# Kernel optimization log

Hardware: AMD Instinct MI355X
Metric: run time of the kernel (lower is better)

The kernel has to match this reference:

```python
import jax, jax.numpy as jnp
import numpy as np

B, NQ, NC1, NC2 = 2, 1024, 1024, 1024
QD = CD1 = CD2 = 1024
H, DH = 8, 64
INNER = H * DH          # 512
VD = 1024               # v_dim, split across heads -> 128 per head
VDH = VD // H


def setup_inputs() -> dict:
    key = jax.random.key(0)
    ks = jax.random.split(key, 18)
    f = lambda k, shape: jax.random.normal(k, shape, jnp.float32) * 0.02
    return {
        "x": f(ks[0], (B, NQ, QD)),
        "context": f(ks[1], (B, NC1, CD1)),
        "context2": f(ks[2], (B, NC2, CD2)),
        "mask1": jax.random.uniform(ks[3], (B, NQ, NC1)) > 0.1,
        "mask2": jax.random.uniform(ks[4], (B, NQ, NC2)) > 0.1,
        "Wq": f(ks[5], (QD, INNER)),  "bq": f(ks[6], (INNER,)),
        "Wk1": f(ks[7], (CD1, INNER)), "bk1": f(ks[8], (INNER,)),
        "Wv1": f(ks[9], (CD1, VD)),    "bv1": f(ks[10], (VD,)),
        "Wk2": f(ks[11], (CD2, INNER)), "bk2": f(ks[12], (INNER,)),
        "Wv2": f(ks[13], (CD2, VD)),    "bv2": f(ks[14], (VD,)),
        "Wo": f(ks[15], (VD, VD)),      "bo": f(ks[16], (VD,)),
    }


def _split_heads(t, d):
    # b n (h d) -> b h n d
    b, n, _ = t.shape
    return t.reshape(b, n, H, d).transpose(0, 2, 1, 3)


def reference(x, context, context2, mask1, mask2,
              Wq, bq, Wk1, bk1, Wv1, bv1, Wk2, bk2, Wv2, bv2, Wo, bo):
    scale = DH ** -0.5
    q = x @ Wq + bq
    k = jnp.concatenate([context @ Wk1 + bk1, context2 @ Wk2 + bk2], axis=1)
    v = jnp.concatenate([context @ Wv1 + bv1, context2 @ Wv2 + bv2], axis=1)

    qh = _split_heads(q, DH)   # [B,H,NQ,DH]
    kh = _split_heads(k, DH)   # [B,H,NC1+NC2,DH]
    vh = _split_heads(v, VDH)  # [B,H,NC1+NC2,VDH]

    sim = jnp.einsum('bhid,bhjd->bhij', qh, kh) * scale  # [B,H,NQ,J]
    mask = jnp.concatenate([mask1, mask2], axis=2)[:, None, :, :]  # [B,1,NQ,J]
    max_neg = -jnp.finfo(sim.dtype).max
    sim = jnp.where(mask, sim, max_neg)

    attn = jax.nn.softmax(sim, axis=-1)
    out = jnp.einsum('bhij,bhjd->bhid', attn, vh)          # [B,H,NQ,VDH]
    out = out.transpose(0, 2, 1, 3).reshape(B, NQ, VD)     # b n (h d)
    return out @ Wo + bo
```

## Files before the change

kernel.cpp:

```cpp
#include <hip/hip_runtime.h>
#include <math.h>

typedef short bf16x8 __attribute__((ext_vector_type(8)));
typedef float f32x4  __attribute__((ext_vector_type(4)));

__device__ __forceinline__ unsigned short f2bf(float f) {
    unsigned int u = __builtin_bit_cast(unsigned int, f);
    u += 0x7FFFu + ((u >> 16) & 1u);
    return (unsigned short)(u >> 16);
}

__device__ __forceinline__ void gld16(const unsigned short* g, unsigned short* l) {
    __builtin_amdgcn_global_load_lds(
        (const __attribute__((address_space(1))) void*)g,
        (__attribute__((address_space(3))) void*)l, 16, 0, 0);
}

__global__ __launch_bounds__(256) void cast3(
    const float* __restrict__ a0, const float* __restrict__ a1, const float* __restrict__ a2,
    unsigned short* __restrict__ o0, unsigned short* __restrict__ o1, unsigned short* __restrict__ o2)
{
    const int z = blockIdx.z;
    const float* a = z == 0 ? a0 : (z == 1 ? a1 : a2);
    unsigned short* o = z == 0 ? o0 : (z == 1 ? o1 : o2);
    size_t i = ((size_t)blockIdx.x * 256 + threadIdx.x) * 8;
    float4 x0 = *(const float4*)&a[i];
    float4 x1 = *(const float4*)&a[i + 4];
    uint4 pk;
    pk.x = (unsigned)f2bf(x0.x) | ((unsigned)f2bf(x0.y) << 16);
    pk.y = (unsigned)f2bf(x0.z) | ((unsigned)f2bf(x0.w) << 16);
    pk.z = (unsigned)f2bf(x1.x) | ((unsigned)f2bf(x1.y) << 16);
    pk.w = (unsigned)f2bf(x1.z) | ((unsigned)f2bf(x1.w) << 16);
    *(uint4*)&o[i] = pk;
}

__global__ __launch_bounds__(256) void cast_t3(
    const float* __restrict__ W0, const float* __restrict__ W1, const float* __restrict__ W2,
    unsigned short* __restrict__ T0, unsigned short* __restrict__ T1, unsigned short* __restrict__ T2,
    int K, int N)
{
    __shared__ float T[64][65];
    const int z = blockIdx.z;
    const float* W = z == 0 ? W0 : (z == 1 ? W1 : W2);
    unsigned short* O = z == 0 ? T0 : (z == 1 ? T1 : T2);
    const int n0 = blockIdx.x << 6, k0 = blockIdx.y << 6;
    const int t = threadIdx.x;
    #pragma unroll
    for (int i = 0; i < 4; i++) {
        int vi = t + (i << 8);
        int r = vi >> 4, c4 = (vi & 15) << 2;
        *(float4*)&T[r][c4] = *(const float4*)&W[(size_t)(k0 + r) * N + n0 + c4];
    }
    __syncthreads();
    #pragma unroll
    for (int i = 0; i < 4; i++) {
        int vi = t + (i << 8);
        int n = vi >> 4, k4 = (vi & 15) << 2;
        uint2 pk;
        pk.x = (unsigned)f2bf(T[k4 + 0][n]) | ((unsigned)f2bf(T[k4 + 1][n]) << 16);
        pk.y = (unsigned)f2bf(T[k4 + 2][n]) | ((unsigned)f2bf(T[k4 + 3][n]) << 16);
        *(uint2*)&O[(size_t)(n0 + n) * K + k0 + k4] = pk;
    }
}

__global__ __launch_bounds__(256) void pack_mask(
    const int* __restrict__ mask1, const int* __restrict__ mask2,
    unsigned long long* __restrict__ mpk)
{
    int wid = (blockIdx.x << 2) + (threadIdx.x >> 6);
    int lane = threadIdx.x & 63;
    const int* m1 = mask1 + ((size_t)wid << 10);
    const int* m2 = mask2 + ((size_t)wid << 10);
    unsigned long long* o = mpk + ((size_t)wid << 5);
    #pragma unroll
    for (int win = 0; win < 16; win++) {
        unsigned long long bal = __ballot(m1[(win << 6) + lane] != 0);
        if (lane == 0) o[win] = bal;
    }
    #pragma unroll
    for (int win = 0; win < 16; win++) {
        unsigned long long bal = __ballot(m2[(win << 6) + lane] != 0);
        if (lane == 0) o[16 + win] = bal;
    }
}

__device__ __forceinline__ void gemm_core(
    const unsigned short* __restrict__ A,
    const unsigned short* __restrict__ Wt,
    int K, int gm0, int gn0,
    unsigned short (*As)[32], unsigned short (*Bs)[32],
    f32x4 (&acc)[4][4])
{
    const int t = threadIdx.x;
    const int lane = t & 63, w = t >> 6;
    const int wm = (w & 1) << 6, wn = (w >> 1) << 6;
    const int l15 = lane & 15, quad = lane >> 4;

    for (int k0 = 0; k0 < K; k0 += 32) {
        __syncthreads();
        #pragma unroll
        for (int i = 0; i < 2; i++) {
            int r0 = (i << 6) + (w << 4);
            int ra = r0 + (lane >> 2);
            int kc = (lane & 3) << 3;
            gld16(&A [(size_t)(gm0 + ra) * K + k0 + kc], &As[r0][0] + ((size_t)lane << 3));
            gld16(&Wt[(size_t)(gn0 + ra) * K + k0 + kc], &Bs[r0][0] + ((size_t)lane << 3));
        }
        __syncthreads();
        bf16x8 af[4], bg[4];
        #pragma unroll
        for (int i = 0; i < 4; i++)
            af[i] = *(const bf16x8*)&As[wm + (i << 4) + l15][quad << 3];
        #pragma unroll
        for (int j = 0; j < 4; j++)
            bg[j] = *(const bf16x8*)&Bs[wn + (j << 4) + l15][quad << 3];
        #pragma unroll
        for (int i = 0; i < 4; i++)
            #pragma unroll
            for (int j = 0; j < 4; j++)
                acc[i][j] = __builtin_amdgcn_mfma_f32_16x16x32_bf16(af[i], bg[j], acc[i][j], 0, 0, 0);
    }
}

__global__ __launch_bounds__(256) void proj_all(
    const unsigned short* __restrict__ xb, const unsigned short* __restrict__ c1b,
    const unsigned short* __restrict__ c2b,
    const unsigned short* __restrict__ Wqt, const unsigned short* __restrict__ Wk1t,
    const unsigned short* __restrict__ Wk2t, const unsigned short* __restrict__ Wv1t,
    const unsigned short* __restrict__ Wv2t,
    const float* __restrict__ bq, const float* __restrict__ bk1, const float* __restrict__ bk2,
    const float* __restrict__ bv1, const float* __restrict__ bv2,
    unsigned short* __restrict__ qbuf, unsigned short* __restrict__ kbuf,
    unsigned short* __restrict__ vbT)
{
    __shared__ unsigned short As[128][32];
    __shared__ unsigned short Bs[128][32];
    const int bid = blockIdx.x;
    int z, bx, by;
    if (bid < 192) { z = bid >> 6; int l = bid & 63; by = l >> 2; bx = l & 3; }
    else { int l = bid - 192; z = 3 + (l >> 7); l &= 127; by = l >> 3; bx = l & 7; }
    const unsigned short* A  = (z == 0) ? xb : (z == 1 || z == 3) ? c1b : c2b;
    const unsigned short* Wt = (z == 0) ? Wqt : (z == 1) ? Wk1t : (z == 2) ? Wk2t
                             : (z == 3) ? Wv1t : Wv2t;
    const float* bias = (z == 0) ? bq : (z == 1) ? bk1 : (z == 2) ? bk2
                      : (z == 3) ? bv1 : bv2;
    const int gm0 = by << 7, gn0 = bx << 7;

    f32x4 acc[4][4];
    #pragma unroll
    for (int i = 0; i < 4; i++)
        #pragma unroll
        for (int j = 0; j < 4; j++) acc[i][j] = (f32x4){0.f, 0.f, 0.f, 0.f};

    gemm_core(A, Wt, 1024, gm0, gn0, As, Bs, acc);

    const int lane = threadIdx.x & 63, w = threadIdx.x >> 6;
    const int wm = (w & 1) << 6, wn = (w >> 1) << 6;
    const int l15 = lane & 15, quad = lane >> 4;
    float bb[4];
    #pragma unroll
    for (int j = 0; j < 4; j++) bb[j] = bias[gn0 + wn + (j << 4) + l15];

    if (z < 3) {
        unsigned short* out = (z == 0) ? qbuf : kbuf;
        const int obs = (z == 0) ? 1024 : 2048;
        const int off = (z == 2) ? 1024 : 0;
        #pragma unroll
        for (int i = 0; i < 4; i++) {
            int mb = gm0 + wm + (i << 4) + (quad << 2);
            #pragma unroll
            for (int p = 0; p < 4; p++) {
                int m = mb + p;
                int orow = ((m >> 10) * obs) + off + (m & 1023);
                #pragma unroll
                for (int j = 0; j < 4; j++)
                    out[(size_t)orow * 512 + gn0 + wn + (j << 4) + l15] = f2bf(acc[i][j][p] + bb[j]);
            }
        }
    } else {
        const int off = (z == 3) ? 0 : 1024;
        #pragma unroll
        for (int i = 0; i < 4; i++) {
            int mb = gm0 + wm + (i << 4) + (quad << 2);
            int b = mb >> 10;
            int jj = (mb & 1023) + off;
            #pragma unroll
            for (int j = 0; j < 4; j++) {
                int n = gn0 + wn + (j << 4) + l15;
                unsigned long long pk = 0;
                #pragma unroll
                for (int p = 0; p < 4; p++)
                    pk |= (unsigned long long)f2bf(acc[i][j][p] + bb[j]) << (16 * p);
                *(unsigned long long*)&vbT[((size_t)b * 1024 + n) * 2048 + jj] = pk;
            }
        }
    }
}

__global__ __launch_bounds__(256) void gemm_out(
    const unsigned short* __restrict__ abuf, const unsigned short* __restrict__ Wot,
    const float* __restrict__ bo, float* __restrict__ out)
{
    __shared__ unsigned short As[128][32];
    __shared__ unsigned short Bs[128][32];
    const int gm0 = blockIdx.y << 7, gn0 = blockIdx.x << 7;

    f32x4 acc[4][4];
    #pragma unroll
    for (int i = 0; i < 4; i++)
        #pragma unroll
        for (int j = 0; j < 4; j++) acc[i][j] = (f32x4){0.f, 0.f, 0.f, 0.f};

    gemm_core(abuf, Wot, 1024, gm0, gn0, As, Bs, acc);

    const int lane = threadIdx.x & 63, w = threadIdx.x >> 6;
    const int wm = (w & 1) << 6, wn = (w >> 1) << 6;
    const int l15 = lane & 15, quad = lane >> 4;
    float bb[4];
    #pragma unroll
    for (int j = 0; j < 4; j++) bb[j] = bo[gn0 + wn + (j << 4) + l15];
    #pragma unroll
    for (int i = 0; i < 4; i++) {
        int mb = gm0 + wm + (i << 4) + (quad << 2);
        #pragma unroll
        for (int p = 0; p < 4; p++)
            #pragma unroll
            for (int j = 0; j < 4; j++)
                out[(size_t)(mb + p) * 1024 + gn0 + wn + (j << 4) + l15] = acc[i][j][p] + bb[j];
    }
}

__global__ __launch_bounds__(256) void attn_mfma(
    const unsigned short* __restrict__ qbuf, const unsigned short* __restrict__ kbuf,
    const unsigned short* __restrict__ vbT, const unsigned long long* __restrict__ mpk,
    float* __restrict__ Opart, float* __restrict__ ml)
{
    __shared__ unsigned short Ks[128][64];
    __shared__ unsigned short VsT[128][128];
    __shared__ unsigned short Ps[64][128];

    const int t = threadIdx.x;
    const int bid = blockIdx.x;
    const int hs = bid >> 8, r = bid & 255;
    const int h = r & 7, qt = (r >> 3) & 15, b = r >> 7;
    const int q0 = qt << 6;
    const int lane = t & 63, w = t >> 6, l15 = lane & 15, quad = lane >> 4;

    const unsigned short* qrow = qbuf + (((size_t)(b << 10) + q0 + (w << 4) + l15) << 9) + (h << 6);
    const bf16x8 aq0 = *(const bf16x8*)&qrow[quad << 3];
    const bf16x8 aq1 = *(const bf16x8*)&qrow[32 + (quad << 3)];

    f32x4 acc[8];
    #pragma unroll
    for (int ct = 0; ct < 8; ct++) acc[ct] = (f32x4){0.f, 0.f, 0.f, 0.f};
    float m_p[4] = {-3.0e38f, -3.0e38f, -3.0e38f, -3.0e38f};
    float l_p[4] = {0.f, 0.f, 0.f, 0.f};

    const size_t kbase = (size_t)b << 20;
    const size_t vbase = ((size_t)((b << 10) + (h << 7))) << 11;
    const int qg = q0 + (w << 4) + (quad << 2);
    const unsigned long long* mrow0 = mpk + (((size_t)(b << 10) + qg) << 5);

    for (int jt = 0; jt < 8; jt++) {
        const int j0 = (hs << 10) + (jt << 7);
        __syncthreads();
        #pragma unroll
        for (int i = 0; i < 4; i++) {
            int vi = t + (i << 8);
            int row = vi >> 3, c = vi & 7;
            *(uint4*)&Ks[row][(c ^ (row & 7)) << 3] =
                *(const uint4*)&kbuf[kbase + ((size_t)(j0 + row) << 9) + (h << 6) + (c << 3)];
        }
        #pragma unroll
        for (int i = 0; i < 8; i++) {
            int vi = t + (i << 8);
            int f = vi >> 4, c = vi & 15;
            int sc = (c & 8) | ((c & 7) ^ (f & 7));
            *(uint4*)&VsT[f][sc << 3] =
                *(const uint4*)&vbT[vbase + ((size_t)f << 11) + j0 + (c << 3)];
        }
        __syncthreads();

        f32x4 s[8];
        #pragma unroll
        for (int n = 0; n < 8; n++) {
            int rowk = (n << 4) + l15;
            bf16x8 bk0 = *(const bf16x8*)&Ks[rowk][(quad ^ (l15 & 7)) << 3];
            bf16x8 bk1 = *(const bf16x8*)&Ks[rowk][((quad | 4) ^ (l15 & 7)) << 3];
            s[n] = (f32x4){0.f, 0.f, 0.f, 0.f};
            s[n] = __builtin_amdgcn_mfma_f32_16x16x32_bf16(aq0, bk0, s[n], 0, 0, 0);
            s[n] = __builtin_amdgcn_mfma_f32_16x16x32_bf16(aq1, bk1, s[n], 0, 0, 0);
        }

        const int wbase = j0 >> 6;
        #pragma unroll
        for (int p = 0; p < 4; p++) {
            const unsigned long long* mr = mrow0 + ((size_t)p << 5);
            unsigned long long w0 = mr[wbase], w1 = mr[wbase + 1];
            #pragma unroll
            for (int n = 0; n < 8; n++) {
                unsigned long long wd = (n < 4) ? w0 : w1;
                int bit = ((n & 3) << 4) + l15;
                float sv = s[n][p] * 0.125f;
                s[n][p] = ((wd >> bit) & 1ull) ? sv : -3.0e38f;
            }
        }

        float alpha[4];
        #pragma unroll
        for (int p = 0; p < 4; p++) {
            float mt = s[0][p];
            #pragma unroll
            for (int n = 1; n < 8; n++) mt = fmaxf(mt, s[n][p]);
            #pragma unroll
            for (int o = 1; o < 16; o <<= 1) mt = fmaxf(mt, __shfl_xor(mt, o, 64));
            float mn = fmaxf(m_p[p], mt);
            float e[8], ls = 0.f;
            #pragma unroll
            for (int n = 0; n < 8; n++) { e[n] = __expf(s[n][p] - mn); ls += e[n]; }
            #pragma unroll
            for (int o = 1; o < 16; o <<= 1) ls += __shfl_xor(ls, o, 64);
            alpha[p] = __expf(m_p[p] - mn);
            l_p[p] = l_p[p] * alpha[p] + ls;
            m_p[p] = mn;
            int pr = (w << 4) + (quad << 2) + p;
            #pragma unroll
            for (int n = 0; n < 8; n++) {
                int c = (n << 1) + (l15 >> 3);
                int sc = (c & 8) | ((c & 7) ^ (pr & 7));
                Ps[pr][(sc << 3) + (l15 & 7)] = f2bf(e[n]);
            }
        }

        #pragma unroll
        for (int ct = 0; ct < 8; ct++)
            #pragma unroll
            for (int p = 0; p < 4; p++) acc[ct][p] *= alpha[p];

        bf16x8 ap[4];
        #pragma unroll
        for (int kk = 0; kk < 4; kk++) {
            int c = (kk << 2) + quad;
            int sc = (c & 8) | ((c & 7) ^ (l15 & 7));
            ap[kk] = *(const bf16x8*)&Ps[(w << 4) + l15][sc << 3];
        }
        #pragma unroll
        for (int ct = 0; ct < 8; ct++) {
            int fv = (ct << 4) + l15;
            #pragma unroll
            for (int kk = 0; kk < 4; kk++) {
                int c = (kk << 2) + quad;
                int sc = (c & 8) | ((c & 7) ^ (l15 & 7));
                bf16x8 bv = *(const bf16x8*)&VsT[fv][sc << 3];
                acc[ct] = __builtin_amdgcn_mfma_f32_16x16x32_bf16(ap[kk], bv, acc[ct], 0, 0, 0);
            }
        }
    }

    #pragma unroll
    for (int p = 0; p < 4; p++) {
        int q = q0 + (w << 4) + (quad << 2) + p;
        size_t idx = (size_t)(hs << 14) + (b << 13) + (h << 10) + q;
        #pragma unroll
        for (int ct = 0; ct < 8; ct++)
            Opart[(idx << 7) + (ct << 4) + l15] = acc[ct][p];
        if (l15 == 0) {
            ml[(idx << 1) + 0] = m_p[p];
            ml[(idx << 1) + 1] = l_p[p];
        }
    }
}

__global__ __launch_bounds__(256) void attn_combine(
    const float* __restrict__ Opart, const float* __restrict__ ml,
    unsigned short* __restrict__ abuf)
{
    int id = (blockIdx.x << 8) + threadIdx.x;
    int bhq = id >> 5, c4 = (id & 31) << 2;
    float2 ml0 = ((const float2*)ml)[bhq];
    float2 ml1 = ((const float2*)ml)[16384 + bhq];
    float M = fmaxf(ml0.x, ml1.x);
    float a0 = __expf(ml0.x - M), a1 = __expf(ml1.x - M);
    float inv = 1.0f / (ml0.y * a0 + ml1.y * a1);
    float4 o0 = *(const float4*)&Opart[((size_t)bhq << 7) + c4];
    float4 o1 = *(const float4*)&Opart[((size_t)(16384 + bhq) << 7) + c4];
    int b = bhq >> 13, hh = (bhq >> 10) & 7, q = bhq & 1023;
    float r0 = (o0.x * a0 + o1.x * a1) * inv;
    float r1 = (o0.y * a0 + o1.y * a1) * inv;
    float r2 = (o0.z * a0 + o1.z * a1) * inv;
    float r3 = (o0.w * a0 + o1.w * a1) * inv;
    unsigned long long pk = (unsigned long long)f2bf(r0)
        | ((unsigned long long)f2bf(r1) << 16)
        | ((unsigned long long)f2bf(r2) << 32)
        | ((unsigned long long)f2bf(r3) << 48);
    *(unsigned long long*)&abuf[((size_t)((b << 10) + q) << 10) + (hh << 7) + c4] = pk;
}

extern "C" void kernel_launch(void* const* d_in, const int* in_sizes, int n_in,
                              void* d_out, int out_size, void* d_ws, size_t ws_size,
                              hipStream_t stream)
{
    const float* x        = (const float*)d_in[0];
    const float* context  = (const float*)d_in[1];
    const float* context2 = (const float*)d_in[2];
    const int*   mask1    = (const int*)d_in[3];
    const int*   mask2    = (const int*)d_in[4];
    const float* Wq  = (const float*)d_in[5];
    const float* bq  = (const float*)d_in[6];
    const float* Wk1 = (const float*)d_in[7];
    const float* bk1 = (const float*)d_in[8];
    const float* Wv1 = (const float*)d_in[9];
    const float* bv1 = (const float*)d_in[10];
    const float* Wk2 = (const float*)d_in[11];
    const float* bk2 = (const float*)d_in[12];
    const float* Wv2 = (const float*)d_in[13];
    const float* bv2 = (const float*)d_in[14];
    const float* Wo  = (const float*)d_in[15];
    const float* bo  = (const float*)d_in[16];
    float* out = (float*)d_out;

    char* W = (char*)d_ws;
    unsigned short* Wot  = (unsigned short*)(W);
    unsigned short* xb   = (unsigned short*)(W + (2ull  << 20));
    unsigned short* c1b  = (unsigned short*)(W + (6ull  << 20));
    unsigned short* c2b  = (unsigned short*)(W + (10ull << 20));
    unsigned short* Wqt  = (unsigned short*)(W + (14ull << 20));
    unsigned short* Wk1t = (unsigned short*)(W + (15ull << 20));
    unsigned short* Wk2t = (unsigned short*)(W + (16ull << 20));
    unsigned short* Wv1t = (unsigned short*)(W + (17ull << 20));
    unsigned short* Wv2t = (unsigned short*)(W + (19ull << 20));
    unsigned short* qbuf = (unsigned short*)(W + (21ull << 20));
    unsigned short* kbuf = (unsigned short*)(W + (23ull << 20));
    unsigned short* vbT  = (unsigned short*)(W + (27ull << 20));
    float*              Opart = (float*)(W + (2ull << 20));
    unsigned long long* mpk   = (unsigned long long*)(W + (18ull << 20));
    float*              mlb   = (float*)(W + (18ull << 20) + (1ull << 19));
    unsigned short*     abuf  = (unsigned short*)(W + (19ull << 20));

    cast3   <<<dim3(1024, 1, 3), 256, 0, stream>>>(x, context, context2, xb, c1b, c2b);
    cast_t3 <<<dim3(8, 16, 3),   256, 0, stream>>>(Wq, Wk1, Wk2, Wqt, Wk1t, Wk2t, 1024, 512);
    cast_t3 <<<dim3(16, 16, 3),  256, 0, stream>>>(Wv1, Wv2, Wo, Wv1t, Wv2t, Wot, 1024, 1024);
    proj_all<<<dim3(448),        256, 0, stream>>>(xb, c1b, c2b, Wqt, Wk1t, Wk2t, Wv1t, Wv2t,
                                                   bq, bk1, bk2, bv1, bv2, qbuf, kbuf, vbT);
    pack_mask<<<dim3(512),       256, 0, stream>>>(mask1, mask2, mpk);
    attn_mfma<<<dim3(512),       256, 0, stream>>>(qbuf, kbuf, vbT, mpk, Opart, mlb);
    attn_combine<<<dim3(2048),   256, 0, stream>>>(Opart, mlb, abuf);
    gemm_out<<<dim3(8, 16),      256, 0, stream>>>(abuf, Wot, bo, out);
}
```

Before: 257.0 us.

## Transpose QK^T MFMA for lane-per-row softmax and narrow output GEMM tiles

The attention kernel swaps the MFMA operands so the S tile comes out transposed. Each lane then holds one query row's scores, so the row max and sum need only two cross-lane shuffles instead of four per row. P is written as packed 64-bit stores into a padded LDS array rather than scattered 16-bit stores, and the per-row rescale factors are fetched by shuffle. Separately, the output-projection GEMM is templated down to 128x64 tiles, doubling its block count to 256 so more CUs are busy, at the cost of more A-tile reloads.

```diff
diff --git a/kernel.cpp b/kernel.cpp
--- a/kernel.cpp
+++ b/kernel.cpp
@@ -84,16 +84,18 @@
     }
 }
 
+template<int NT>
 __device__ __forceinline__ void gemm_core(
     const unsigned short* __restrict__ A,
     const unsigned short* __restrict__ Wt,
     int K, int gm0, int gn0,
     unsigned short (*As)[32], unsigned short (*Bs)[32],
-    f32x4 (&acc)[4][4])
-{
+    f32x4 (&acc)[4][NT / 32])
+{
+    constexpr int NS = NT / 32;
     const int t = threadIdx.x;
     const int lane = t & 63, w = t >> 6;
-    const int wm = (w & 1) << 6, wn = (w >> 1) << 6;
+    const int wm = (w & 1) << 6, wn = (w >> 1) * (NT / 2);
     const int l15 = lane & 15, quad = lane >> 4;
 
     for (int k0 = 0; k0 < K; k0 += 32) {
@@ -103,21 +105,27 @@
             int r0 = (i << 6) + (w << 4);
             int ra = r0 + (lane >> 2);
             int kc = (lane & 3) << 3;
-            gld16(&A [(size_t)(gm0 + ra) * K + k0 + kc], &As[r0][0] + ((size_t)lane << 3));
+            gld16(&A[(size_t)(gm0 + ra) * K + k0 + kc], &As[r0][0] + ((size_t)lane << 3));
+        }
+        #pragma unroll
+        for (int i = 0; i < NT / 64; i++) {
+            int r0 = (i << 6) + (w << 4);
+            int ra = r0 + (lane >> 2);
+            int kc = (lane & 3) << 3;
             gld16(&Wt[(size_t)(gn0 + ra) * K + k0 + kc], &Bs[r0][0] + ((size_t)lane << 3));
         }
         __syncthreads();
-        bf16x8 af[4], bg[4];
+        bf16x8 af[4], bg[NS];
         #pragma unroll
         for (int i = 0; i < 4; i++)
             af[i] = *(const bf16x8*)&As[wm + (i << 4) + l15][quad << 3];
         #pragma unroll
-        for (int j = 0; j < 4; j++)
+        for (int j = 0; j < NS; j++)
             bg[j] = *(const bf16x8*)&Bs[wn + (j << 4) + l15][quad << 3];
         #pragma unroll
         for (int i = 0; i < 4; i++)
             #pragma unroll
-            for (int j = 0; j < 4; j++)
+            for (int j = 0; j < NS; j++)
                 acc[i][j] = __builtin_amdgcn_mfma_f32_16x16x32_bf16(af[i], bg[j], acc[i][j], 0, 0, 0);
     }
 }
@@ -152,7 +160,7 @@
         #pragma unroll
         for (int j = 0; j < 4; j++) acc[i][j] = (f32x4){0.f, 0.f, 0.f, 0.f};
 
-    gemm_core(A, Wt, 1024, gm0, gn0, As, Bs, acc);
+    gemm_core<128>(A, Wt, 1024, gm0, gn0, As, Bs, acc);
 
     const int lane = threadIdx.x & 63, w = threadIdx.x >> 6;
     const int wm = (w & 1) << 6, wn = (w >> 1) << 6;
@@ -202,30 +210,30 @@
     const float* __restrict__ bo, float* __restrict__ out)
 {
     __shared__ unsigned short As[128][32];
-    __shared__ unsigned short Bs[128][32];
-    const int gm0 = blockIdx.y << 7, gn0 = blockIdx.x << 7;
-
-    f32x4 acc[4][4];
+    __shared__ unsigned short Bs[64][32];
+    const int gm0 = blockIdx.y << 7, gn0 = blockIdx.x << 6;
+
+    f32x4 acc[4][2];
     #pragma unroll
     for (int i = 0; i < 4; i++)
         #pragma unroll
-        for (int j = 0; j < 4; j++) acc[i][j] = (f32x4){0.f, 0.f, 0.f, 0.f};
-
-    gemm_core(abuf, Wot, 1024, gm0, gn0, As, Bs, acc);
+        for (int j = 0; j < 2; j++) acc[i][j] = (f32x4){0.f, 0.f, 0.f, 0.f};
+
+    gemm_core<64>(abuf, Wot, 1024, gm0, gn0, As, Bs, acc);
 
     const int lane = threadIdx.x & 63, w = threadIdx.x >> 6;
-    const int wm = (w & 1) << 6, wn = (w >> 1) << 6;
+    const int wm = (w & 1) << 6, wn = (w >> 1) << 5;
     const int l15 = lane & 15, quad = lane >> 4;
-    float bb[4];
-    #pragma unroll
-    for (int j = 0; j < 4; j++) bb[j] = bo[gn0 + wn + (j << 4) + l15];
+    float bb[2];
+    #pragma unroll
+    for (int j = 0; j < 2; j++) bb[j] = bo[gn0 + wn + (j << 4) + l15];
     #pragma unroll
     for (int i = 0; i < 4; i++) {
         int mb = gm0 + wm + (i << 4) + (quad << 2);
         #pragma unroll
         for (int p = 0; p < 4; p++)
             #pragma unroll
-            for (int j = 0; j < 4; j++)
+            for (int j = 0; j < 2; j++)
                 out[(size_t)(mb + p) * 1024 + gn0 + wn + (j << 4) + l15] = acc[i][j][p] + bb[j];
     }
 }
@@ -237,7 +245,7 @@
 {
     __shared__ unsigned short Ks[128][64];
     __shared__ unsigned short VsT[128][128];
-    __shared__ unsigned short Ps[64][128];
+    __shared__ unsigned short Ps[64][132];
 
     const int t = threadIdx.x;
     const int bid = blockIdx.x;
@@ -253,13 +261,11 @@
     f32x4 acc[8];
     #pragma unroll
     for (int ct = 0; ct < 8; ct++) acc[ct] = (f32x4){0.f, 0.f, 0.f, 0.f};
-    float m_p[4] = {-3.0e38f, -3.0e38f, -3.0e38f, -3.0e38f};
-    float l_p[4] = {0.f, 0.f, 0.f, 0.f};
+    float m_l = -3.0e38f, l_l = 0.f;
 
     const size_t kbase = (size_t)b << 20;
     const size_t vbase = ((size_t)((b << 10) + (h << 7))) << 11;
-    const int qg = q0 + (w << 4) + (quad << 2);
-    const unsigned long long* mrow0 = mpk + (((size_t)(b << 10) + qg) << 5);
+    const unsigned long long* mrow = mpk + (((size_t)(b << 10) + q0 + (w << 4) + l15) << 5);
 
     for (int jt = 0; jt < 8; jt++) {
         const int j0 = (hs << 10) + (jt << 7);
@@ -288,71 +294,71 @@
             bf16x8 bk0 = *(const bf16x8*)&Ks[rowk][(quad ^ (l15 & 7)) << 3];
             bf16x8 bk1 = *(const bf16x8*)&Ks[rowk][((quad | 4) ^ (l15 & 7)) << 3];
             s[n] = (f32x4){0.f, 0.f, 0.f, 0.f};
-            s[n] = __builtin_amdgcn_mfma_f32_16x16x32_bf16(aq0, bk0, s[n], 0, 0, 0);
-            s[n] = __builtin_amdgcn_mfma_f32_16x16x32_bf16(aq1, bk1, s[n], 0, 0, 0);
+            s[n] = __builtin_amdgcn_mfma_f32_16x16x32_bf16(bk0, aq0, s[n], 0, 0, 0);
+            s[n] = __builtin_amdgcn_mfma_f32_16x16x32_bf16(bk1, aq1, s[n], 0, 0, 0);
         }
 
         const int wbase = j0 >> 6;
-        #pragma unroll
-        for (int p = 0; p < 4; p++) {
-            const unsigned long long* mr = mrow0 + ((size_t)p << 5);
-            unsigned long long w0 = mr[wbase], w1 = mr[wbase + 1];
-            #pragma unroll
-            for (int n = 0; n < 8; n++) {
-                unsigned long long wd = (n < 4) ? w0 : w1;
-                int bit = ((n & 3) << 4) + l15;
+        const unsigned long long w0 = mrow[wbase], w1 = mrow[wbase + 1];
+        #pragma unroll
+        for (int n = 0; n < 8; n++) {
+            unsigned long long wd = (n < 4) ? w0 : w1;
+            int bit0 = ((n & 3) << 4) + (quad << 2);
+            #pragma unroll
+            for (int p = 0; p < 4; p++) {
                 float sv = s[n][p] * 0.125f;
-                s[n][p] = ((wd >> bit) & 1ull) ? sv : -3.0e38f;
+                s[n][p] = ((wd >> (bit0 + p)) & 1ull) ? sv : -3.0e38f;
             }
         }
 
-        float alpha[4];
-        #pragma unroll
-        for (int p = 0; p < 4; p++) {
-            float mt = s[0][p];
-            #pragma unroll
-            for (int n = 1; n < 8; n++) mt = fmaxf(mt, s[n][p]);
-            #pragma unroll
-            for (int o = 1; o < 16; o <<= 1) mt = fmaxf(mt, __shfl_xor(mt, o, 64));
-            float mn = fmaxf(m_p[p], mt);
-            float e[8], ls = 0.f;
-            #pragma unroll
-            for (int n = 0; n < 8; n++) { e[n] = __expf(s[n][p] - mn); ls += e[n]; }
-            #pragma unroll
-            for (int o = 1; o < 16; o <<= 1) ls += __shfl_xor(ls, o, 64);
-            alpha[p] = __expf(m_p[p] - mn);
-            l_p[p] = l_p[p] * alpha[p] + ls;
-            m_p[p] = mn;
-            int pr = (w << 4) + (quad << 2) + p;
-            #pragma unroll
-            for (int n = 0; n < 8; n++) {
-                int c = (n << 1) + (l15 >> 3);
-                int sc = (c & 8) | ((c & 7) ^ (pr & 7));
-                Ps[pr][(sc << 3) + (l15 & 7)] = f2bf(e[n]);
-            }
-        }
-
+        float mt = s[0][0];
+        #pragma unroll
+        for (int n = 0; n < 8; n++)
+            #pragma unroll
+            for (int p = 0; p < 4; p++) mt = fmaxf(mt, s[n][p]);
+        mt = fmaxf(mt, __shfl_xor(mt, 16, 64));
+        mt = fmaxf(mt, __shfl_xor(mt, 32, 64));
+        float mn = fmaxf(m_l, mt);
+        float ls = 0.f;
+        #pragma unroll
+        for (int n = 0; n < 8; n++) {
+            float e0 = __expf(s[n][0] - mn), e1 = __expf(s[n][1] - mn);
+            float e2 = __expf(s[n][2] - mn), e3 = __expf(s[n][3] - mn);
+            ls += (e0 + e1) + (e2 + e3);
+            unsigned long long pk = (unsigned long long)f2bf(e0)
+                | ((unsigned long long)f2bf(e1) << 16)
+                | ((unsigned long long)f2bf(e2) << 32)
+                | ((unsigned long long)f2bf(e3) << 48);
+            *(unsigned long long*)&Ps[(w << 4) + l15][(n << 4) + (quad << 2)] = pk;
+        }
+        ls += __shfl_xor(ls, 16, 64);
+        ls += __shfl_xor(ls, 32, 64);
+        float al = __expf(m_l - mn);
+        l_l = l_l * al + ls;
+        m_l = mn;
+
+        float ar[4];
+        #pragma unroll
+        for (int p = 0; p < 4; p++)
+            ar[p] = __shfl(al, (lane & 48) | ((quad << 2) + p), 64);
         #pragma unroll
         for (int ct = 0; ct < 8; ct++)
             #pragma unroll
-            for (int p = 0; p < 4; p++) acc[ct][p] *= alpha[p];
+            for (int p = 0; p < 4; p++) acc[ct][p] *= ar[p];
 
         bf16x8 ap[4];
         #pragma unroll
-        for (int kk = 0; kk < 4; kk++) {
-            int c = (kk << 2) + quad;
-            int sc = (c & 8) | ((c & 7) ^ (l15 & 7));
-            ap[kk] = *(const bf16x8*)&Ps[(w << 4) + l15][sc << 3];
-        }
+        for (int win = 0; win < 4; win++)
+            ap[win] = *(const bf16x8*)&Ps[(w << 4) + l15][(win << 5) + (quad << 3)];
         #pragma unroll
         for (int ct = 0; ct < 8; ct++) {
             int fv = (ct << 4) + l15;
             #pragma unroll
-            for (int kk = 0; kk < 4; kk++) {
-                int c = (kk << 2) + quad;
+            for (int win = 0; win < 4; win++) {
+                int c = (win << 2) + quad;
                 int sc = (c & 8) | ((c & 7) ^ (l15 & 7));
                 bf16x8 bv = *(const bf16x8*)&VsT[fv][sc << 3];
-                acc[ct] = __builtin_amdgcn_mfma_f32_16x16x32_bf16(ap[kk], bv, acc[ct], 0, 0, 0);
+                acc[ct] = __builtin_amdgcn_mfma_f32_16x16x32_bf16(ap[win], bv, acc[ct], 0, 0, 0);
             }
         }
     }
@@ -364,10 +370,12 @@
         #pragma unroll
         for (int ct = 0; ct < 8; ct++)
             Opart[(idx << 7) + (ct << 4) + l15] = acc[ct][p];
-        if (l15 == 0) {
-            ml[(idx << 1) + 0] = m_p[p];
-            ml[(idx << 1) + 1] = l_p[p];
-        }
+    }
+    if (quad == 0) {
+        int q = q0 + (w << 4) + l15;
+        size_t idx = (size_t)(hs << 14) + (b << 13) + (h << 10) + q;
+        ml[(idx << 1) + 0] = m_l;
+        ml[(idx << 1) + 1] = l_l;
     }
 }
 
@@ -445,5 +453,5 @@
     pack_mask<<<dim3(512),       256, 0, stream>>>(mask1, mask2, mpk);
     attn_mfma<<<dim3(512),       256, 0, stream>>>(qbuf, kbuf, vbT, mpk, Opart, mlb);
     attn_combine<<<dim3(2048),   256, 0, stream>>>(Opart, mlb, abuf);
-    gemm_out<<<dim3(8, 16),      256, 0, stream>>>(abuf, Wot, bo, out);
-}
+    gemm_out<<<dim3(16, 16),     256, 0, stream>>>(abuf, Wot, bo, out);
+}
```

Result: faster. 240.2 us (-6.5%).
